# Kernel tuning notes

Hardware: AMD Instinct MI355X
Metric: run time of the kernel (lower is better)

The kernel has to match this reference:

```python
import jax, jax.numpy as jnp
import numpy as np

B, N, C = 8, 4096, 768
H = 12
D = C // H  # 64


def setup_inputs() -> dict:
    key = jax.random.key(0)
    k1, k2, k3 = jax.random.split(key, 3)
    x = jax.random.normal(k1, (B, N, C), dtype=jnp.float32)
    Wqkv = jax.random.normal(k2, (C, 3 * C), dtype=jnp.float32) * (C ** -0.5)
    Wproj = jax.random.normal(k3, (C, C), dtype=jnp.float32) * (C ** -0.5)
    bproj = jnp.zeros((C,), dtype=jnp.float32)
    return {"x": x, "Wqkv": Wqkv, "Wproj": Wproj, "bproj": bproj}


def reference(x, Wqkv, Wproj, bproj):
    b, n, c = x.shape
    qkv = x @ Wqkv  # [B,N,3C]
    qkv = qkv.reshape(b, n, 3, H, D).transpose(2, 0, 3, 1, 4)  # [3,B,H,N,D]
    q, k, v = qkv[0], qkv[1], qkv[2]
    # softmax over the sequence axis (dim=-2 in torch => N)
    k = jax.nn.softmax(k, axis=-2)
    # context: [B,H,D,D] -- small d x d intermediate
    context = jnp.einsum('bhnd,bhne->bhde', k, v)
    out = jnp.einsum('bhnd,bhde->bhne', q, context)  # [B,H,N,D]
    out = out.transpose(0, 2, 1, 3).reshape(b, n, c)  # b h n d -> b n (h d)
    return out @ Wproj + bproj
```

## Files before the change

### kernel.cpp

```cpp
#include <hip/hip_runtime.h>
#include <cstdint>
#include <cstddef>


typedef __bf16 bf8_t __attribute__((ext_vector_type(8)));
typedef float f4_t __attribute__((ext_vector_type(4)));
typedef float f16_t __attribute__((ext_vector_type(16)));

#define DEV_INLINE __device__ __forceinline__

DEV_INLINE void gload16(const void* g, void* l) {
  __builtin_amdgcn_global_load_lds(
      (const __attribute__((address_space(1))) void*)g,
      (__attribute__((address_space(3))) void*)l, 16, 0, 0);
}

__global__ __launch_bounds__(256) void cast_f32_bf16(const float* __restrict__ in,
                                                     __bf16* __restrict__ out, int n4) {
  int i = blockIdx.x * 256 + threadIdx.x;
  if (i >= n4) return;
  float4 f = ((const float4*)in)[i];
  union { __bf16 h[4]; uint2 u; } o;
  o.h[0] = (__bf16)f.x; o.h[1] = (__bf16)f.y; o.h[2] = (__bf16)f.z; o.h[3] = (__bf16)f.w;
  ((uint2*)out)[i] = o.u;
}

__global__ __launch_bounds__(256) void transpose_cast(const float* __restrict__ in,
                                                      __bf16* __restrict__ out, int R, int C) {
  __shared__ float t[64][65];
  const int tilesR = R >> 6;
  const int tr = blockIdx.x % tilesR, tc = blockIdx.x / tilesR;
  const int tx = threadIdx.x & 63, ty = threadIdx.x >> 6;
  const int r0 = tr * 64, c0 = tc * 64;
#pragma unroll
  for (int p = 0; p < 16; p++) {
    int r = p * 4 + ty;
    t[r][tx] = in[(size_t)(r0 + r) * C + c0 + tx];
  }
  __syncthreads();
#pragma unroll
  for (int p = 0; p < 16; p++) {
    int c = p * 4 + ty;
    out[(size_t)(c0 + c) * R + r0 + tx] = (__bf16)t[tx][c];
  }
}

__global__ __launch_bounds__(256) void wq_cast(const float* __restrict__ in,
                                               __bf16* __restrict__ out) {
  int o = blockIdx.x * 256 + threadIdx.x;
  int r = o / 768, c = o - r * 768;
  out[o] = (__bf16)in[r * 2304 + c];
}


#define MFMA32(aa, bb, cc) cc = __builtin_amdgcn_mfma_f32_32x32x16_bf16(aa, bb, cc, 0, 0, 0)

#define SAu(d, u, kc) gload16(gA + (size_t)((u) * 64) * 768 + (kc),           \
                              sA + (d) * 16384 + (u) * 4096 + tid * 8)
#define SBu(d, u, kc) gload16(gB + (size_t)((u) * 64) * 768 + (kc),           \
                              sB + (d) * 16384 + (u) * 4096 + tid * 8)

#define G_SETUP()                                                             \
  const int tid = threadIdx.x;                                                \
  const int gcol = ((tid & 7) ^ ((tid >> 3) & 7)) * 8;                        \
  const int lane = tid & 63, wv = tid >> 6;                                   \
  const int wm = wv >> 2, wn = wv & 3;                                        \
  const int l31 = lane & 31, l5 = lane >> 5, key = lane & 7;                  \
  const int kof0 = ((0 | l5) ^ key) * 8;                                      \
  const int kof1 = ((2 | l5) ^ key) * 8;                                      \
  const int kof2 = ((4 | l5) ^ key) * 8;                                      \
  const int kof3 = ((6 | l5) ^ key) * 8;                                      \
  const int rowA = (wm * 128 + l31) * 64;                                     \
  const int rowB = (wn * 64 + l31) * 64;                                      \
  f16_t acc[4][2];                                                            \
  _Pragma("unroll") for (int i_ = 0; i_ < 4; i_++)                            \
    _Pragma("unroll") for (int j_ = 0; j_ < 2; j_++)                          \
      _Pragma("unroll") for (int e_ = 0; e_ < 16; e_++) acc[i_][j_][e_] = 0.f;

#define G_TILE(SA_STAGE, SB_STAGE) do {                                       \
    const __bf16* aBp = sA + cur * 16384;                                     \
    const __bf16* bBp = sB + cur * 16384;                                     \
    bf8_t a0x, a1x, a2x, a3x, a0y, a1y, a2y, a3y, bq0, bq1;                   \
                                              \
    a0x = *(const bf8_t*)(aBp + rowA +        kof0);                          \
    a1x = *(const bf8_t*)(aBp + rowA + 2048 + kof0);                          \
    a2x = *(const bf8_t*)(aBp + rowA + 4096 + kof0);                          \
    a3x = *(const bf8_t*)(aBp + rowA + 6144 + kof0);                          \
    a0y = *(const bf8_t*)(aBp + rowA +        kof1);                          \
    a1y = *(const bf8_t*)(aBp + rowA + 2048 + kof1);                          \
    a2y = *(const bf8_t*)(aBp + rowA + 4096 + kof1);                          \
    a3y = *(const bf8_t*)(aBp + rowA + 6144 + kof1);                          \
    bq0 = *(const bf8_t*)(bBp + rowB + kof0);                                 \
    bq1 = *(const bf8_t*)(bBp + rowB + kof1);                                 \
    SA_STAGE;                                                                 \
    __builtin_amdgcn_s_barrier();                                             \
    __builtin_amdgcn_s_setprio(1);                                            \
    MFMA32(a0x, bq0, acc[0][0]); MFMA32(a0y, bq1, acc[0][0]);                 \
    MFMA32(a1x, bq0, acc[1][0]); MFMA32(a1y, bq1, acc[1][0]);                 \
    MFMA32(a2x, bq0, acc[2][0]); MFMA32(a2y, bq1, acc[2][0]);                 \
    MFMA32(a3x, bq0, acc[3][0]); MFMA32(a3y, bq1, acc[3][0]);                 \
    __builtin_amdgcn_s_setprio(0);                                            \
    __builtin_amdgcn_s_barrier();                                             \
                                                 \
    bq0 = *(const bf8_t*)(bBp + rowB + 2048 + kof0);                          \
    bq1 = *(const bf8_t*)(bBp + rowB + 2048 + kof1);                          \
    SB_STAGE;                                                                 \
    __builtin_amdgcn_s_barrier();                                             \
    __builtin_amdgcn_s_setprio(1);                                            \
    MFMA32(a0x, bq0, acc[0][1]); MFMA32(a0y, bq1, acc[0][1]);                 \
    MFMA32(a1x, bq0, acc[1][1]); MFMA32(a1y, bq1, acc[1][1]);                 \
    MFMA32(a2x, bq0, acc[2][1]); MFMA32(a2y, bq1, acc[2][1]);                 \
    MFMA32(a3x, bq0, acc[3][1]); MFMA32(a3y, bq1, acc[3][1]);                 \
    __builtin_amdgcn_s_setprio(0);                                            \
    __builtin_amdgcn_s_barrier();                                             \
                                              \
    a0x = *(const bf8_t*)(aBp + rowA +        kof2);                          \
    a1x = *(const bf8_t*)(aBp + rowA + 2048 + kof2);                          \
    a2x = *(const bf8_t*)(aBp + rowA + 4096 + kof2);                          \
    a3x = *(const bf8_t*)(aBp + rowA + 6144 + kof2);                          \
    a0y = *(const bf8_t*)(aBp + rowA +        kof3);                          \
    a1y = *(const bf8_t*)(aBp + rowA + 2048 + kof3);                          \
    a2y = *(const bf8_t*)(aBp + rowA + 4096 + kof3);                          \
    a3y = *(const bf8_t*)(aBp + rowA + 6144 + kof3);                          \
    bq0 = *(const bf8_t*)(bBp + rowB + kof2);                                 \
    bq1 = *(const bf8_t*)(bBp + rowB + kof3);                                 \
    __builtin_amdgcn_s_barrier();                                             \
    __builtin_amdgcn_s_setprio(1);                                            \
    MFMA32(a0x, bq0, acc[0][0]); MFMA32(a0y, bq1, acc[0][0]);                 \
    MFMA32(a1x, bq0, acc[1][0]); MFMA32(a1y, bq1, acc[1][0]);                 \
    MFMA32(a2x, bq0, acc[2][0]); MFMA32(a2y, bq1, acc[2][0]);                 \
    MFMA32(a3x, bq0, acc[3][0]); MFMA32(a3y, bq1, acc[3][0]);                 \
    __builtin_amdgcn_s_setprio(0);                                            \
    __builtin_amdgcn_s_barrier();                                             \
                                                         \
    bq0 = *(const bf8_t*)(bBp + rowB + 2048 + kof2);                          \
    bq1 = *(const bf8_t*)(bBp + rowB + 2048 + kof3);                          \
    __builtin_amdgcn_s_barrier();                                             \
    __builtin_amdgcn_s_setprio(1);                                            \
    MFMA32(a0x, bq0, acc[0][1]); MFMA32(a0y, bq1, acc[0][1]);                 \
    MFMA32(a1x, bq0, acc[1][1]); MFMA32(a1y, bq1, acc[1][1]);                 \
    MFMA32(a2x, bq0, acc[2][1]); MFMA32(a2y, bq1, acc[2][1]);                 \
    MFMA32(a3x, bq0, acc[3][1]); MFMA32(a3y, bq1, acc[3][1]);                 \
    __builtin_amdgcn_s_setprio(0);                                            \
    __syncthreads();          \
  } while (0)

#define G_MAIN() do {                                                         \
    SAu(0, 0, 0); SAu(0, 1, 0); SAu(0, 2, 0); SAu(0, 3, 0);                   \
    SBu(0, 0, 0); SBu(0, 1, 0); SBu(0, 2, 0); SBu(0, 3, 0);                   \
    __syncthreads();                                                          \
    int cur = 0;                                                              \
    for (int t = 0; t < 11; ++t) {                                            \
      const int kcn = (t + 1) * 64;                                           \
      const int nx = cur ^ 1;                                                 \
      G_TILE({ SAu(nx, 0, kcn); SAu(nx, 1, kcn);                              \
               SAu(nx, 2, kcn); SAu(nx, 3, kcn); },                           \
             { SBu(nx, 0, kcn); SBu(nx, 1, kcn);                              \
               SBu(nx, 2, kcn); SBu(nx, 3, kcn); });                          \
      cur = nx;                                                               \
    }                                                                         \
    G_TILE({}, {});                                                           \
  } while (0)

__global__ __launch_bounds__(512, 2) void gemm1_kv(const __bf16* __restrict__ A,
                                                   const __bf16* __restrict__ B,
                                                   __bf16* __restrict__ KTo,
                                                   __bf16* __restrict__ VTo) {
  __shared__ __bf16 sA[2 * 16384];
  __shared__ __bf16 sB[2 * 16384];
  const int xcd = blockIdx.x & 7, g = blockIdx.x >> 3;
  const int mt = xcd * 16 + g / 6, nt = g % 6;
  G_SETUP();
  const __bf16* gA = A + (size_t)(mt * 256 + (tid >> 3)) * 768 + gcol;
  const __bf16* gB = B + (size_t)(nt * 256 + (tid >> 3)) * 768 + gcol;

  G_MAIN();

  const int sKV = (nt >= 3);
  __bf16* T = sKV ? VTo : KTo;
  const int bb = mt >> 4;
  const int tok0 = (mt & 15) * 256 + wm * 128 + 4 * l5;
  const int cbase = (nt - sKV * 3) * 256 + wn * 64;
#pragma unroll
  for (int m = 0; m < 4; m++) {
#pragma unroll
    for (int n = 0; n < 2; n++) {
      int c = cbase + n * 32 + l31;
      __bf16* Tp = T + ((size_t)(bb * 12 + (c >> 6)) * 64 + (c & 63)) * 4096;
      int tk = tok0 + m * 32;
#pragma unroll
      for (int q = 0; q < 4; q++) {
        union { __bf16 h4[4]; uint2 u2; } pk;
#pragma unroll
        for (int r = 0; r < 4; r++) pk.h4[r] = (__bf16)acc[m][n][q * 4 + r];
        *(uint2*)&Tp[tk + 8 * q] = pk.u2;
      }
    }
  }
}

__global__ __launch_bounds__(256) void stats_rows(const __bf16* __restrict__ KT,
                                                  float2* __restrict__ stats) {
  __shared__ float red[8];
  const __bf16* p = KT + (size_t)blockIdx.x * 4096;
  const int tid = threadIdx.x, lane = tid & 63, wv = tid >> 6;
  bf8_t x0 = *(const bf8_t*)&p[tid * 16];
  bf8_t x1 = *(const bf8_t*)&p[tid * 16 + 8];
  float v[16];
#pragma unroll
  for (int k = 0; k < 8; k++) { v[k] = (float)x0[k]; v[8 + k] = (float)x1[k]; }
  float m = v[0];
#pragma unroll
  for (int k = 1; k < 16; k++) m = fmaxf(m, v[k]);
  for (int o = 32; o; o >>= 1) m = fmaxf(m, __shfl_xor(m, o, 64));
  if (lane == 0) red[wv] = m;
  __syncthreads();
  m = fmaxf(fmaxf(red[0], red[1]), fmaxf(red[2], red[3]));
  float s = 0.f;
#pragma unroll
  for (int k = 0; k < 16; k++) s += __expf(v[k] - m);
  for (int o = 32; o; o >>= 1) s += __shfl_xor(s, o, 64);
  if (lane == 0) red[4 + wv] = s;
  __syncthreads();
  if (tid == 0) {
    float st = red[4] + red[5] + red[6] + red[7];
    stats[blockIdx.x] = make_float2(m, 1.0f / st);
  }
}

__global__ __launch_bounds__(256) void ctx_kernel(const __bf16* __restrict__ KT,
                                                  const __bf16* __restrict__ VT,
                                                  const float2* __restrict__ stats,
                                                  float* __restrict__ part) {
  const int bh = blockIdx.x >> 3, kc = blockIdx.x & 7;
  const int tid = threadIdx.x, lane = tid & 63, wv = tid >> 6;
  const int wr = (wv >> 1) * 32, wc = (wv & 1) * 32;
  const int lr = lane & 15, quad = lane >> 4;
  const __bf16* Ab = KT + (size_t)bh * 64 * 4096;
  const __bf16* Bb = VT + (size_t)bh * 64 * 4096;
  float2 st[2];
  st[0] = stats[bh * 64 + wr + lr];
  st[1] = stats[bh * 64 + wr + 16 + lr];
  const f4_t fz = {0.f, 0.f, 0.f, 0.f};
  f4_t acc[2][2] = {{fz, fz}, {fz, fz}};
  const int kbeg = kc * 512;
  for (int k0 = kbeg; k0 < kbeg + 512; k0 += 32) {
    bf8_t a[2], b[2];
#pragma unroll
    for (int i = 0; i < 2; i++) {
      bf8_t raw = *(const bf8_t*)&Ab[(size_t)(wr + i * 16 + lr) * 4096 + k0 + quad * 8];
#pragma unroll
      for (int e = 0; e < 8; e++)
        a[i][e] = (__bf16)(__expf((float)raw[e] - st[i].x) * st[i].y);
    }
#pragma unroll
    for (int j = 0; j < 2; j++)
      b[j] = *(const bf8_t*)&Bb[(size_t)(wc + j * 16 + lr) * 4096 + k0 + quad * 8];
#pragma unroll
    for (int i = 0; i < 2; i++)
#pragma unroll
      for (int j = 0; j < 2; j++)
        acc[i][j] = __builtin_amdgcn_mfma_f32_16x16x32_bf16(a[i], b[j], acc[i][j], 0, 0, 0);
  }
  float* po = part + (size_t)blockIdx.x * 4096;
#pragma unroll
  for (int i = 0; i < 2; i++)
#pragma unroll
    for (int j = 0; j < 2; j++)
#pragma unroll
      for (int r = 0; r < 4; r++)
        po[(wr + i * 16 + quad * 4 + r) * 64 + wc + j * 16 + lr] = acc[i][j][r];
}

__global__ __launch_bounds__(256) void wfused_kernel(const float* __restrict__ part,
                                                     const __bf16* __restrict__ WpT,
                                                     __bf16* __restrict__ B2T) {
  __shared__ __bf16 sctx[64 * 64];
  const int bh = blockIdx.x, cblk = blockIdx.y;
  const int b = bh / 12, h = bh % 12;
  const int tid = threadIdx.x;
  for (int i = tid; i < 4096; i += 256) {
    float s = 0.f;
#pragma unroll
    for (int kc = 0; kc < 8; kc++) s += part[(size_t)(bh * 8 + kc) * 4096 + i];
    sctx[i] = (__bf16)s;
  }
  __syncthreads();
  const int lane = tid & 63, wv = tid >> 6, lr = lane & 15, quad = lane >> 4;
  const int c0 = cblk * 192 + wv * 48;
  const f4_t fz = {0.f, 0.f, 0.f, 0.f};
  f4_t acc[3][4];
#pragma unroll
  for (int i = 0; i < 3; i++)
#pragma unroll
    for (int j = 0; j < 4; j++) acc[i][j] = fz;
#pragma unroll
  for (int k0 = 0; k0 < 64; k0 += 32) {
    bf8_t a[3], bq[4];
#pragma unroll
    for (int i = 0; i < 3; i++)
      a[i] = *(const bf8_t*)&WpT[(size_t)(c0 + i * 16 + lr) * 768 + h * 64 + k0 + quad * 8];
#pragma unroll
    for (int j = 0; j < 4; j++)
      bq[j] = *(const bf8_t*)&sctx[(j * 16 + lr) * 64 + k0 + quad * 8];
#pragma unroll
    for (int i = 0; i < 3; i++)
#pragma unroll
      for (int j = 0; j < 4; j++)
        acc[i][j] = __builtin_amdgcn_mfma_f32_16x16x32_bf16(a[i], bq[j], acc[i][j], 0, 0, 0);
  }
#pragma unroll
  for (int i = 0; i < 3; i++)
#pragma unroll
    for (int j = 0; j < 4; j++)
#pragma unroll
      for (int r = 0; r < 4; r++) {
        int c = c0 + i * 16 + quad * 4 + r;
        int d = j * 16 + lr;
        B2T[((size_t)b * 768 + c) * 768 + h * 64 + d] = (__bf16)acc[i][j][r];
      }
}

__global__ __launch_bounds__(256) void combine_kernel(const __bf16* __restrict__ B2Tall,
                                                      const __bf16* __restrict__ Wq,
                                                      __bf16* __restrict__ Wcomb) {
  constexpr int LD = 768, BK = 32, KTOT = 768;
  __shared__ __bf16 sAc[64 * 32];
  __shared__ __bf16 sBc[64 * 32];
  const int b = blockIdx.x / 144, rem = blockIdx.x % 144;
  const int mt = rem / 12, nt = rem % 12;
  const __bf16* A = B2Tall + (size_t)b * 768 * 768;
  const int tid = threadIdx.x, lane = tid & 63, wv = tid >> 6;
  const int wr = (wv >> 1) * 32, wc = (wv & 1) * 32;
  const int lr = lane & 15, quad = lane >> 4;

  const int e0 = tid * 8;
  const int srow = e0 >> 5, skk = e0 & 31;
  const __bf16* gA = A + (size_t)(mt * 64 + srow) * LD + skk;
  const __bf16* gB = Wq + (size_t)(nt * 64 + srow) * LD + skk;

  const f4_t fz = {0.f, 0.f, 0.f, 0.f};
  f4_t acc[2][2] = {{fz, fz}, {fz, fz}};

  for (int k0 = 0; k0 < KTOT; k0 += BK) {
    gload16(gA, &sAc[e0]);
    gload16(gB, &sBc[e0]);
    gA += BK; gB += BK;
    __syncthreads();
    bf8_t a[2], bq[2];
#pragma unroll
    for (int i = 0; i < 2; i++)
      a[i] = *(const bf8_t*)&sAc[(wr + i * 16 + lr) * 32 + quad * 8];
#pragma unroll
    for (int j = 0; j < 2; j++)
      bq[j] = *(const bf8_t*)&sBc[(wc + j * 16 + lr) * 32 + quad * 8];
#pragma unroll
    for (int i = 0; i < 2; i++)
#pragma unroll
      for (int j = 0; j < 2; j++)
        acc[i][j] = __builtin_amdgcn_mfma_f32_16x16x32_bf16(a[i], bq[j], acc[i][j], 0, 0, 0);
    __syncthreads();
  }
  __bf16* C = Wcomb + (size_t)b * 768 * 768;
  const int row0 = mt * 64 + wr, col0 = nt * 64 + wc;
#pragma unroll
  for (int i = 0; i < 2; i++)
#pragma unroll
    for (int j = 0; j < 2; j++)
#pragma unroll
      for (int r = 0; r < 4; r++)
        C[(size_t)(row0 + i * 16 + quad * 4 + r) * 768 + col0 + j * 16 + lr] =
            (__bf16)acc[i][j][r];
}

__global__ __launch_bounds__(512, 2) void gemm2_out(const __bf16* __restrict__ A,
                                                    const __bf16* __restrict__ Ball,
                                                    float* __restrict__ C,
                                                    const float* __restrict__ bias) {
  __shared__ __bf16 sA[2 * 16384];
  __shared__ __bf16 sB[2 * 16384];
  const int xcd = blockIdx.x & 7, g = blockIdx.x >> 3;
  const int mt = xcd * 16 + g / 3, nt = g % 3;
  const __bf16* B = Ball + (size_t)(mt >> 4) * 768 * 768;
  G_SETUP();
  const __bf16* gA = A + (size_t)(mt * 256 + (tid >> 3)) * 768 + gcol;
  const __bf16* gB = B + (size_t)(nt * 256 + (tid >> 3)) * 768 + gcol;

  G_MAIN();

  const int row0 = mt * 256 + wm * 128 + 4 * l5;
  const int col0 = nt * 256 + wn * 64;
#pragma unroll
  for (int m = 0; m < 4; m++) {
#pragma unroll
    for (int n = 0; n < 2; n++) {
      int col = col0 + n * 32 + l31;
      float bv = bias[col];
#pragma unroll
      for (int q = 0; q < 4; q++) {
        int rb = row0 + m * 32 + 8 * q;
#pragma unroll
        for (int r = 0; r < 4; r++)
          C[(size_t)(rb + r) * 768 + col] = acc[m][n][q * 4 + r] + bv;
      }
    }
  }
}

extern "C" void kernel_launch(void* const* d_in, const int* in_sizes, int n_in,
                              void* d_out, int out_size, void* d_ws, size_t ws_size,
                              hipStream_t stream) {
  const float* x = (const float*)d_in[0];
  const float* Wqkv = (const float*)d_in[1];
  const float* Wproj = (const float*)d_in[2];
  const float* bproj = (const float*)d_in[3];
  float* out = (float*)d_out;

  char* ws = (char*)d_ws;
  __bf16* Xb    = (__bf16*)(ws + 0);
  __bf16* KT    = (__bf16*)(ws + 50331648);
  __bf16* VT    = (__bf16*)(ws + 100663296);
  __bf16* WqkvT = (__bf16*)(ws + 150994944);
  float2* stats = (float2*)(ws + 150994944);
  __bf16* Wqc   = (__bf16*)(ws + 154533888);
  __bf16* WpT   = (__bf16*)(ws + 155713536);
  float*  part  = (float*)(ws + 156893184);
  __bf16* B2T   = (__bf16*)(ws + 169476096);
  __bf16* Wcomb = (__bf16*)(ws + 178913280);

  cast_f32_bf16<<<24576, 256, 0, stream>>>(x, Xb, 25165824 / 4);
  transpose_cast<<<12 * 36, 256, 0, stream>>>(Wqkv, WqkvT, 768, 2304);
  wq_cast<<<(768 * 768) / 256, 256, 0, stream>>>(Wqkv, Wqc);
  transpose_cast<<<12 * 12, 256, 0, stream>>>(Wproj, WpT, 768, 768);
  gemm1_kv<<<768, 512, 0, stream>>>(Xb, WqkvT + 768 * 768, KT, VT);
  stats_rows<<<6144, 256, 0, stream>>>(KT, stats);
  ctx_kernel<<<96 * 8, 256, 0, stream>>>(KT, VT, stats, part);
  wfused_kernel<<<dim3(96, 4), 256, 0, stream>>>(part, WpT, B2T);
  combine_kernel<<<1152, 256, 0, stream>>>(B2T, Wqc, Wcomb);
  gemm2_out<<<384, 512, 0, stream>>>(Xb, Wcomb, out, bproj);
}
```

Before: 411.2 us.

## Switch GEMM mainloop to 4-stage BK=32 pipeline with explicit vmcnt waits

Restructures the shared GEMM mainloop used by gemm1_kv and gemm2_out. It drops from a double-buffered BK=64 tile to a four-deep ring of BK=32 tiles, prefetching three tiles ahead. Completion is tracked with explicit s_waitcnt vmcnt/lgkmcnt instead of a full __syncthreads per tile. The LDS swizzle and global row mapping are adjusted for 32-wide rows. This is meant to hide global-load latency better, at the cost of more barriers per K element and more fragile manual wait-count bookkeeping.

```diff
diff --git a/kernel.cpp b/kernel.cpp
--- a/kernel.cpp
+++ b/kernel.cpp
@@ -55,124 +55,99 @@
 
 #define MFMA32(aa, bb, cc) cc = __builtin_amdgcn_mfma_f32_32x32x16_bf16(aa, bb, cc, 0, 0, 0)
 
-#define SAu(d, u, kc) gload16(gA + (size_t)((u) * 64) * 768 + (kc),           \
-                              sA + (d) * 16384 + (u) * 4096 + tid * 8)
-#define SBu(d, u, kc) gload16(gB + (size_t)((u) * 64) * 768 + (kc),           \
-                              sB + (d) * 16384 + (u) * 4096 + tid * 8)
+#define SAu(d, u, kc) gload16(gA + (size_t)((u) * 128) * 768 + (kc),          \
+                              sA + (d) * 8192 + (u) * 4096 + tid * 8)
+#define SBu(d, u, kc) gload16(gB + (size_t)((u) * 128) * 768 + (kc),          \
+                              sB + (d) * 8192 + (u) * 4096 + tid * 8)
+#define STAGE_T(d, kc) do { SAu(d,0,kc); SAu(d,1,kc); SBu(d,0,kc); SBu(d,1,kc); } while (0)
 
 #define G_SETUP()                                                             \
   const int tid = threadIdx.x;                                                \
-  const int gcol = ((tid & 7) ^ ((tid >> 3) & 7)) * 8;                        \
+  const int srow = tid >> 2;                                                  \
+  const int gcol = ((tid & 3) ^ ((srow >> 1) & 3)) * 8;                       \
   const int lane = tid & 63, wv = tid >> 6;                                   \
   const int wm = wv >> 2, wn = wv & 3;                                        \
-  const int l31 = lane & 31, l5 = lane >> 5, key = lane & 7;                  \
-  const int kof0 = ((0 | l5) ^ key) * 8;                                      \
-  const int kof1 = ((2 | l5) ^ key) * 8;                                      \
-  const int kof2 = ((4 | l5) ^ key) * 8;                                      \
-  const int kof3 = ((6 | l5) ^ key) * 8;                                      \
-  const int rowA = (wm * 128 + l31) * 64;                                     \
-  const int rowB = (wn * 64 + l31) * 64;                                      \
+  const int l31 = lane & 31, l5 = lane >> 5;                                  \
+  const int key = (l31 >> 1) & 3;                                             \
+  const int kof0 = ((0 | l5) ^ key) * 8;                       \
+  const int kof1 = ((2 | l5) ^ key) * 8;                       \
+  const int rowA = (wm * 128 + l31) * 32;             \
+  const int rowB = (wn * 64 + l31) * 32;              \
   f16_t acc[4][2];                                                            \
   _Pragma("unroll") for (int i_ = 0; i_ < 4; i_++)                            \
     _Pragma("unroll") for (int j_ = 0; j_ < 2; j_++)                          \
       _Pragma("unroll") for (int e_ = 0; e_ < 16; e_++) acc[i_][j_][e_] = 0.f;
 
-#define G_TILE(SA_STAGE, SB_STAGE) do {                                       \
-    const __bf16* aBp = sA + cur * 16384;                                     \
-    const __bf16* bBp = sB + cur * 16384;                                     \
-    bf8_t a0x, a1x, a2x, a3x, a0y, a1y, a2y, a3y, bq0, bq1;                   \
-                                              \
-    a0x = *(const bf8_t*)(aBp + rowA +        kof0);                          \
-    a1x = *(const bf8_t*)(aBp + rowA + 2048 + kof0);                          \
-    a2x = *(const bf8_t*)(aBp + rowA + 4096 + kof0);                          \
-    a3x = *(const bf8_t*)(aBp + rowA + 6144 + kof0);                          \
-    a0y = *(const bf8_t*)(aBp + rowA +        kof1);                          \
-    a1y = *(const bf8_t*)(aBp + rowA + 2048 + kof1);                          \
-    a2y = *(const bf8_t*)(aBp + rowA + 4096 + kof1);                          \
-    a3y = *(const bf8_t*)(aBp + rowA + 6144 + kof1);                          \
-    bq0 = *(const bf8_t*)(bBp + rowB + kof0);                                 \
-    bq1 = *(const bf8_t*)(bBp + rowB + kof1);                                 \
+#define G_TILE(SA_STAGE, SB_STAGE, TAILV) do {                                \
+    const __bf16* aBp = sA + cur * 8192;                                      \
+    const __bf16* bBp = sB + cur * 8192;                                      \
+    bf8_t a00, a01, a10, a11, a20, a21, a30, a31, b0, b1;                     \
+    a00 = *(const bf8_t*)(aBp + rowA +        kof0);                          \
+    a01 = *(const bf8_t*)(aBp + rowA +        kof1);                          \
+    a10 = *(const bf8_t*)(aBp + rowA + 1024 + kof0);                          \
+    a11 = *(const bf8_t*)(aBp + rowA + 1024 + kof1);                          \
+    a20 = *(const bf8_t*)(aBp + rowA + 2048 + kof0);                          \
+    a21 = *(const bf8_t*)(aBp + rowA + 2048 + kof1);                          \
+    a30 = *(const bf8_t*)(aBp + rowA + 3072 + kof0);                          \
+    a31 = *(const bf8_t*)(aBp + rowA + 3072 + kof1);                          \
+    b0  = *(const bf8_t*)(bBp + rowB + kof0);                                 \
+    b1  = *(const bf8_t*)(bBp + rowB + kof1);                                 \
     SA_STAGE;                                                                 \
     __builtin_amdgcn_s_barrier();                                             \
+    asm volatile("s_waitcnt lgkmcnt(0)" ::: "memory");                        \
     __builtin_amdgcn_s_setprio(1);                                            \
-    MFMA32(a0x, bq0, acc[0][0]); MFMA32(a0y, bq1, acc[0][0]);                 \
-    MFMA32(a1x, bq0, acc[1][0]); MFMA32(a1y, bq1, acc[1][0]);                 \
-    MFMA32(a2x, bq0, acc[2][0]); MFMA32(a2y, bq1, acc[2][0]);                 \
-    MFMA32(a3x, bq0, acc[3][0]); MFMA32(a3y, bq1, acc[3][0]);                 \
+    MFMA32(a00, b0, acc[0][0]); MFMA32(a01, b1, acc[0][0]);                   \
+    MFMA32(a10, b0, acc[1][0]); MFMA32(a11, b1, acc[1][0]);                   \
+    MFMA32(a20, b0, acc[2][0]); MFMA32(a21, b1, acc[2][0]);                   \
+    MFMA32(a30, b0, acc[3][0]); MFMA32(a31, b1, acc[3][0]);                   \
     __builtin_amdgcn_s_setprio(0);                                            \
     __builtin_amdgcn_s_barrier();                                             \
-                                                 \
-    bq0 = *(const bf8_t*)(bBp + rowB + 2048 + kof0);                          \
-    bq1 = *(const bf8_t*)(bBp + rowB + 2048 + kof1);                          \
+    b0 = *(const bf8_t*)(bBp + rowB + 1024 + kof0);                           \
+    b1 = *(const bf8_t*)(bBp + rowB + 1024 + kof1);                           \
     SB_STAGE;                                                                 \
     __builtin_amdgcn_s_barrier();                                             \
+    asm volatile("s_waitcnt lgkmcnt(0)" ::: "memory");                        \
     __builtin_amdgcn_s_setprio(1);                                            \
-    MFMA32(a0x, bq0, acc[0][1]); MFMA32(a0y, bq1, acc[0][1]);                 \
-    MFMA32(a1x, bq0, acc[1][1]); MFMA32(a1y, bq1, acc[1][1]);                 \
-    MFMA32(a2x, bq0, acc[2][1]); MFMA32(a2y, bq1, acc[2][1]);                 \
-    MFMA32(a3x, bq0, acc[3][1]); MFMA32(a3y, bq1, acc[3][1]);                 \
+    MFMA32(a00, b0, acc[0][1]); MFMA32(a01, b1, acc[0][1]);                   \
+    MFMA32(a10, b0, acc[1][1]); MFMA32(a11, b1, acc[1][1]);                   \
+    MFMA32(a20, b0, acc[2][1]); MFMA32(a21, b1, acc[2][1]);                   \
+    MFMA32(a30, b0, acc[3][1]); MFMA32(a31, b1, acc[3][1]);                   \
     __builtin_amdgcn_s_setprio(0);                                            \
+    TAILV;                                                                    \
     __builtin_amdgcn_s_barrier();                                             \
-                                              \
-    a0x = *(const bf8_t*)(aBp + rowA +        kof2);                          \
-    a1x = *(const bf8_t*)(aBp + rowA + 2048 + kof2);                          \
-    a2x = *(const bf8_t*)(aBp + rowA + 4096 + kof2);                          \
-    a3x = *(const bf8_t*)(aBp + rowA + 6144 + kof2);                          \
-    a0y = *(const bf8_t*)(aBp + rowA +        kof3);                          \
-    a1y = *(const bf8_t*)(aBp + rowA + 2048 + kof3);                          \
-    a2y = *(const bf8_t*)(aBp + rowA + 4096 + kof3);                          \
-    a3y = *(const bf8_t*)(aBp + rowA + 6144 + kof3);                          \
-    bq0 = *(const bf8_t*)(bBp + rowB + kof2);                                 \
-    bq1 = *(const bf8_t*)(bBp + rowB + kof3);                                 \
+  } while (0)
+
+#define G_MAIN() do {                                                         \
+    STAGE_T(0, 0); STAGE_T(1, 32); STAGE_T(2, 64);                            \
+    asm volatile("s_waitcnt vmcnt(8)" ::: "memory");                          \
     __builtin_amdgcn_s_barrier();                                             \
-    __builtin_amdgcn_s_setprio(1);                                            \
-    MFMA32(a0x, bq0, acc[0][0]); MFMA32(a0y, bq1, acc[0][0]);                 \
-    MFMA32(a1x, bq0, acc[1][0]); MFMA32(a1y, bq1, acc[1][0]);                 \
-    MFMA32(a2x, bq0, acc[2][0]); MFMA32(a2y, bq1, acc[2][0]);                 \
-    MFMA32(a3x, bq0, acc[3][0]); MFMA32(a3y, bq1, acc[3][0]);                 \
-    __builtin_amdgcn_s_setprio(0);                                            \
-    __builtin_amdgcn_s_barrier();                                             \
-                                                         \
-    bq0 = *(const bf8_t*)(bBp + rowB + 2048 + kof2);                          \
-    bq1 = *(const bf8_t*)(bBp + rowB + 2048 + kof3);                          \
-    __builtin_amdgcn_s_barrier();                                             \
-    __builtin_amdgcn_s_setprio(1);                                            \
-    MFMA32(a0x, bq0, acc[0][1]); MFMA32(a0y, bq1, acc[0][1]);                 \
-    MFMA32(a1x, bq0, acc[1][1]); MFMA32(a1y, bq1, acc[1][1]);                 \
-    MFMA32(a2x, bq0, acc[2][1]); MFMA32(a2y, bq1, acc[2][1]);                 \
-    MFMA32(a3x, bq0, acc[3][1]); MFMA32(a3y, bq1, acc[3][1]);                 \
-    __builtin_amdgcn_s_setprio(0);                                            \
-    __syncthreads();          \
-  } while (0)
-
-#define G_MAIN() do {                                                         \
-    SAu(0, 0, 0); SAu(0, 1, 0); SAu(0, 2, 0); SAu(0, 3, 0);                   \
-    SBu(0, 0, 0); SBu(0, 1, 0); SBu(0, 2, 0); SBu(0, 3, 0);                   \
-    __syncthreads();                                                          \
     int cur = 0;                                                              \
-    for (int t = 0; t < 11; ++t) {                                            \
-      const int kcn = (t + 1) * 64;                                           \
-      const int nx = cur ^ 1;                                                 \
-      G_TILE({ SAu(nx, 0, kcn); SAu(nx, 1, kcn);                              \
-               SAu(nx, 2, kcn); SAu(nx, 3, kcn); },                           \
-             { SBu(nx, 0, kcn); SBu(nx, 1, kcn);                              \
-               SBu(nx, 2, kcn); SBu(nx, 3, kcn); });                          \
-      cur = nx;                                                               \
+    for (int t = 0; t < 21; ++t) {                                            \
+      const int nx = (cur + 3) & 3;                                           \
+      const int kcn = (t + 3) * 32;                                           \
+      G_TILE({ SAu(nx, 0, kcn); SAu(nx, 1, kcn); },                           \
+             { SBu(nx, 0, kcn); SBu(nx, 1, kcn); },                           \
+             { asm volatile("s_waitcnt vmcnt(8)" ::: "memory"); });           \
+      cur = (cur + 1) & 3;                                                    \
     }                                                                         \
-    G_TILE({}, {});                                                           \
+    G_TILE({}, {}, { asm volatile("s_waitcnt vmcnt(4)" ::: "memory"); });     \
+    cur = (cur + 1) & 3;                                                      \
+    G_TILE({}, {}, { asm volatile("s_waitcnt vmcnt(0)" ::: "memory"); });     \
+    cur = (cur + 1) & 3;                                                      \
+    G_TILE({}, {}, {});                                                       \
   } while (0)
 
 __global__ __launch_bounds__(512, 2) void gemm1_kv(const __bf16* __restrict__ A,
                                                    const __bf16* __restrict__ B,
                                                    __bf16* __restrict__ KTo,
                                                    __bf16* __restrict__ VTo) {
-  __shared__ __bf16 sA[2 * 16384];
-  __shared__ __bf16 sB[2 * 16384];
+  __shared__ __bf16 sA[4 * 8192];
+  __shared__ __bf16 sB[4 * 8192];
   const int xcd = blockIdx.x & 7, g = blockIdx.x >> 3;
   const int mt = xcd * 16 + g / 6, nt = g % 6;
   G_SETUP();
-  const __bf16* gA = A + (size_t)(mt * 256 + (tid >> 3)) * 768 + gcol;
-  const __bf16* gB = B + (size_t)(nt * 256 + (tid >> 3)) * 768 + gcol;
+  const __bf16* gA = A + (size_t)(mt * 256 + srow) * 768 + gcol;
+  const __bf16* gB = B + (size_t)(nt * 256 + srow) * 768 + gcol;
 
   G_MAIN();
 
@@ -377,14 +352,14 @@
                                                     const __bf16* __restrict__ Ball,
                                                     float* __restrict__ C,
                                                     const float* __restrict__ bias) {
-  __shared__ __bf16 sA[2 * 16384];
-  __shared__ __bf16 sB[2 * 16384];
+  __shared__ __bf16 sA[4 * 8192];
+  __shared__ __bf16 sB[4 * 8192];
   const int xcd = blockIdx.x & 7, g = blockIdx.x >> 3;
   const int mt = xcd * 16 + g / 3, nt = g % 3;
   const __bf16* B = Ball + (size_t)(mt >> 4) * 768 * 768;
   G_SETUP();
-  const __bf16* gA = A + (size_t)(mt * 256 + (tid >> 3)) * 768 + gcol;
-  const __bf16* gB = B + (size_t)(nt * 256 + (tid >> 3)) * 768 + gcol;
+  const __bf16* gA = A + (size_t)(mt * 256 + srow) * 768 + gcol;
+  const __bf16* gB = B + (size_t)(nt * 256 + srow) * 768 + gcol;
 
   G_MAIN();
 
```

Result: no change. 407.3 us (-0.9%).
